# Kernel optimization log

Hardware: AMD Instinct MI355X
Metric: run time of the kernel (lower is better)

## Reference

```python
import jax, jax.numpy as jnp
import numpy as np

N = 100000   # nodes
E = 1200000  # edges
IN = 128     # in_channels
H = 64       # hidden_channels


def setup_inputs() -> dict:
    key = jax.random.key(0)
    ks = jax.random.split(key, 8)
    x = jax.random.normal(ks[0], (N, IN), jnp.float32)
    edge_index = jax.random.randint(ks[1], (2, E), 0, N, dtype=jnp.int32)
    W_pre = jax.random.normal(ks[2], (IN, H), jnp.float32) * (1.0 / np.sqrt(IN))
    b_pre = jnp.zeros((H,), jnp.float32)
    W1 = jax.random.normal(ks[3], (H, H), jnp.float32) * (1.0 / np.sqrt(H))
    b1 = jnp.zeros((H,), jnp.float32)
    W2 = jax.random.normal(ks[4], (H, H), jnp.float32) * (1.0 / np.sqrt(H))
    b2 = jnp.zeros((H,), jnp.float32)
    return {"x": x, "edge_index": edge_index, "W_pre": W_pre, "b_pre": b_pre,
            "W1": W1, "b1": b1, "W2": W2, "b2": b2}


def _gcn_conv(x, src, dst, W, b, n):
    # PyG GCNConv: x' = D^{-1/2} (A + I) D^{-1/2} (x @ W) + b
    x = x @ W                                   # [N, H]
    deg = jax.ops.segment_sum(jnp.ones_like(dst, jnp.float32), dst, num_segments=n)
    dinv = jnp.where(deg > 0, jax.lax.rsqrt(jnp.maximum(deg, 1e-12)), 0.0)
    norm = dinv[src] * dinv[dst]                # [E+N]
    msg = x[src] * norm[:, None]                # gather + scale, [E+N, H]
    out = jax.ops.segment_sum(msg, dst, num_segments=n)  # scatter-add, [N, H]
    return out + b


def reference(x, edge_index, W_pre, b_pre, W1, b1, W2, b2):
    n = x.shape[0]
    loop = jnp.arange(n, dtype=edge_index.dtype)
    # add self-loops once (same structure both layers)
    src = jnp.concatenate([edge_index[0], loop])
    dst = jnp.concatenate([edge_index[1], loop])
    x = x @ W_pre + b_pre
    ori_x = x
    x = jax.nn.relu(_gcn_conv(x, src, dst, W1, b1, n))
    x = jax.nn.relu(_gcn_conv(x, src, dst, W2, b2, n))
    return (x, ori_x)
```

## Files before the change

kernel.cpp:

```cpp
#include <hip/hip_runtime.h>

#define H 64
#define SLOTS 64
#define NPB 128
#define BSHIFT 7
#define CAP 2048
#define CHUNK 4096
#define CPAD 16

typedef __attribute__((ext_vector_type(8))) short short8;
typedef __attribute__((ext_vector_type(4))) float floatx4;
typedef __attribute__((ext_vector_type(8))) unsigned short ushort8v;

static __device__ __forceinline__ unsigned short f2bf(float f) {
  union { float f; unsigned u; } x{f};
  unsigned r = x.u + 0x7fffu + ((x.u >> 16) & 1u);
  return (unsigned short)(r >> 16);
}
static __device__ __forceinline__ float bf2f(unsigned short u) {
  union { unsigned u; float f; } x{(unsigned)u << 16};
  return x.f;
}


__global__ __launch_bounds__(512) void bucket_scatter_kernel(const int* __restrict__ src,
                                                             const int* __restrict__ dst,
                                                             int* __restrict__ gcursor,
                                                             unsigned int* __restrict__ bpk,
                                                             int E, int NB) {
  __shared__ int cnt[1024];
  __shared__ int base[1024];
  int t = threadIdx.x;
  for (int i = t; i < NB; i += 512) cnt[i] = 0;
  __syncthreads();
  int cbase = blockIdx.x * CHUNK;
  int s[CHUNK / 512], d[CHUNK / 512];
#pragma unroll
  for (int j = 0; j < CHUNK / 512; ++j) {
    int e = cbase + j * 512 + t;
    s[j] = (e < E) ? src[e] : -1;
    d[j] = (e < E) ? dst[e] : -1;
    if (d[j] >= 0) atomicAdd(&cnt[d[j] >> BSHIFT], 1);
  }
  __syncthreads();
  for (int i = t; i < NB; i += 512)
    base[i] = cnt[i] ? (i * CAP + atomicAdd(&gcursor[i * CPAD], cnt[i])) : 0;
  __syncthreads();
  for (int i = t; i < NB; i += 512) cnt[i] = 0;
  __syncthreads();
#pragma unroll
  for (int j = 0; j < CHUNK / 512; ++j) {
    if (d[j] >= 0) {
      int b = d[j] >> BSHIFT;
      int r = atomicAdd(&cnt[b], 1);
      int slot = base[b] + r;
      if (slot < (b + 1) * CAP)
        bpk[slot] = ((unsigned)s[j] << BSHIFT) | (unsigned)(d[j] & (NPB - 1));
    }
  }
}


__global__ __launch_bounds__(256) void slab_build_kernel(const unsigned int* __restrict__ bpk,
                                                         const int* __restrict__ gcursor,
                                                         int* __restrict__ csr64,
                                                         float* __restrict__ dinv, int N) {
  __shared__ int cnt[NPB];
  __shared__ int woff[NPB];
  const int b = blockIdx.x;
  const int t = threadIdx.x;
  if (t < NPB) cnt[t] = 0;
  __syncthreads();
  const int beg = b * CAP;
  const int end = beg + min(gcursor[b * CPAD], CAP);
  for (int e = beg + t; e < end; e += 256)
    atomicAdd(&cnt[bpk[e] & (NPB - 1)], 1);
  __syncthreads();

  if (t < NPB) {
    int node = b * NPB + t;
    if (node < N) {
      csr64[(size_t)node * SLOTS] = cnt[t];
      dinv[node] = rsqrtf((float)cnt[t] + 1.0f);
    }
    woff[t] = 0;
  }
  __syncthreads();

  for (int e = beg + t; e < end; e += 256) {
    unsigned pk = bpk[e];
    int nl = (int)(pk & (NPB - 1));
    int r = atomicAdd(&woff[nl], 1);
    if (r < SLOTS - 1)
      csr64[((size_t)(b * NPB + nl)) * SLOTS + 1 + r] = (int)(pk >> BSHIFT);
  }
}


__global__ __launch_bounds__(256) void wprep_kernel(const float* __restrict__ Wpre,
                                                    const float* __restrict__ W1,
                                                    const float* __restrict__ W2,
                                                    unsigned short* __restrict__ frag) {
  int i = blockIdx.x * 256 + threadIdx.x;
  const float* W;
  int K, base;
  if (i < 8192) {
    W = Wpre; K = 128; base = 0;
  } else if (i < 12288) {
    W = W1; K = 64; base = 8192;
  } else if (i < 16384) {
    W = W2; K = 64; base = 12288;
  } else {
    return;
  }
  int s = i - base;
  int j = s & 7;
  int t = s >> 3;
  int l = t & 63;
  int t2 = t >> 6;
  int KB = K / 32;
  int kb = t2 % KB;
  int w = t2 / KB;
  int k = kb * 32 + ((l >> 4) & 3) * 8 + j;
  int n = w * 16 + (l & 15);
  frag[i] = f2bf(W[k * H + n]);
}


__global__ __launch_bounds__(256) void fused_gemm_kernel(
    const float* __restrict__ X, const unsigned short* __restrict__ Wfrag,
    const float* __restrict__ bpre, const float* __restrict__ dinv,
    float* __restrict__ ori, unsigned short* __restrict__ g, int N) {
  __shared__ __align__(16) unsigned short As[4 * 64 * 8];
  __shared__ __align__(16) unsigned short os[16 * 72];
  __shared__ float dinv_s[16];
  const int tid = threadIdx.x;
  const int w = tid >> 6;
  const int lane = tid & 63;
  const int row0 = blockIdx.x * 16;

  {
    int kb = tid >> 6;
    int l = tid & 63;
    int m = l & 15;
    int k0 = kb * 32 + (l >> 4) * 8;
    int r = row0 + m;
    ushort8v v = {0, 0, 0, 0, 0, 0, 0, 0};
    if (r < N) {
      const float* xp = &X[(size_t)r * 128 + k0];
      float4 a = *(const float4*)xp;
      float4 b = *(const float4*)(xp + 4);
      v = ushort8v{f2bf(a.x), f2bf(a.y), f2bf(a.z), f2bf(a.w),
                   f2bf(b.x), f2bf(b.y), f2bf(b.z), f2bf(b.w)};
    }
    *(ushort8v*)&As[(kb * 64 + l) * 8] = v;
  }
  if (tid < 16) dinv_s[tid] = (row0 + tid < N) ? dinv[row0 + tid] : 1.f;

  short8 bfragP[4], bfrag1[2];
  {
    const unsigned short* wf = &Wfrag[((size_t)(w * 4) * 64 + lane) * 8];
#pragma unroll
    for (int kb = 0; kb < 4; ++kb) bfragP[kb] = *(const short8*)&wf[kb * 512];
    const unsigned short* wf1 = &Wfrag[8192 + ((size_t)(w * 2) * 64 + lane) * 8];
#pragma unroll
    for (int kb = 0; kb < 2; ++kb) bfrag1[kb] = *(const short8*)&wf1[kb * 512];
  }
  __syncthreads();

  floatx4 accP = {0.f, 0.f, 0.f, 0.f};
#pragma unroll
  for (int kb = 0; kb < 4; ++kb) {
    short8 a = *(const short8*)&As[(kb * 64 + lane) * 8];
    accP = __builtin_amdgcn_mfma_f32_16x16x32_bf16(a, bfragP[kb], accP, 0, 0, 0);
  }

  const int c = w * 16 + (lane & 15);
  const int q = lane >> 4;
  {
    float bv = bpre[c];
#pragma unroll
    for (int r = 0; r < 4; ++r) {
      int m = q * 4 + r;
      int row = row0 + m;
      float v = accP[r] + bv;
      if (row < N) ori[(size_t)row * H + c] = v;
      os[m * 72 + c] = f2bf(v);
    }
  }
  __syncthreads();

  floatx4 acc2 = {0.f, 0.f, 0.f, 0.f};
#pragma unroll
  for (int kb = 0; kb < 2; ++kb) {
    short8 a = *(const short8*)&os[(lane & 15) * 72 + kb * 32 + (lane >> 4) * 8];
    acc2 = __builtin_amdgcn_mfma_f32_16x16x32_bf16(a, bfrag1[kb], acc2, 0, 0, 0);
  }
#pragma unroll
  for (int r = 0; r < 4; ++r) {
    int row = row0 + q * 4 + r;
    if (row < N) g[(size_t)row * H + c] = f2bf(acc2[r] * dinv_s[q * 4 + r]);
  }
}


static __device__ __forceinline__ float gather_rows(const unsigned short* __restrict__ g,
                                                    int hv, int deg, int lane, int zrow) {
  float acc = 0.f;
#pragma unroll
  for (int b = 0; b < 4; ++b) {
    if (b * 16 < deg) {
      float x[16];
#pragma unroll
      for (int u = 0; u < 16; ++u) {
        int slot = b * 16 + 1 + u;
        int sidx = (slot < SLOTS) ? __builtin_amdgcn_readlane(hv, slot) : zrow;
        sidx = (slot <= deg) ? sidx : zrow;
        x[u] = bf2f(g[(size_t)sidx * H + lane]);
      }
#pragma unroll
      for (int u = 0; u < 16; ++u) acc += x[u];
    }
  }
  return acc;
}


__global__ __launch_bounds__(1024) void gather_fused_kernel(
    const unsigned short* __restrict__ g, const int* __restrict__ csr64,
    const float* __restrict__ bias, const unsigned short* __restrict__ w2frag,
    unsigned short* __restrict__ out, int N) {
  __shared__ __align__(16) unsigned short os[16 * 72];
  __shared__ float dinv_s[16];
  const int tid = threadIdx.x;
  const int w = tid >> 6;
  const int lane = tid & 63;
  const int node0 = blockIdx.x * 16;
  const int node = node0 + w;

  float x1 = 0.f;
  if (node < N) {
    int hv = csr64[(size_t)node * SLOTS + lane];
    float self = bf2f(g[(size_t)node * H + lane]);
    float bl = bias[lane];
    int degt = __builtin_amdgcn_readlane(hv, 0);
    float dn = rsqrtf((float)degt + 1.0f);
    int deg = min(degt, SLOTS - 1);
    float acc = self + gather_rows(g, hv, deg, lane, N);
    x1 = fmaxf(fmaf(dn, acc, bl), 0.f);
    if (lane == 0) dinv_s[w] = dn;
  }
  os[w * 72 + lane] = f2bf(x1);
  __syncthreads();

  if (w < 4) {
    short8 bfrag[2];
#pragma unroll
    for (int kb = 0; kb < 2; ++kb)
      bfrag[kb] = *(const short8*)&w2frag[((size_t)(w * 2 + kb) * 64 + lane) * 8];
    floatx4 acc2 = {0.f, 0.f, 0.f, 0.f};
#pragma unroll
    for (int kb = 0; kb < 2; ++kb) {
      short8 a = *(const short8*)&os[(lane & 15) * 72 + kb * 32 + (lane >> 4) * 8];
      acc2 = __builtin_amdgcn_mfma_f32_16x16x32_bf16(a, bfrag[kb], acc2, 0, 0, 0);
    }
    const int c = w * 16 + (lane & 15);
    const int q = lane >> 4;
#pragma unroll
    for (int r = 0; r < 4; ++r) {
      int row = node0 + q * 4 + r;
      if (row < N) out[(size_t)row * H + c] = f2bf(acc2[r] * dinv_s[q * 4 + r]);
    }
  }
}


__global__ __launch_bounds__(256) void gather_kernel(const unsigned short* __restrict__ g,
                                                     const int* __restrict__ csr64,
                                                     const float* __restrict__ bias,
                                                     float* __restrict__ out, int N) {
  int node = (blockIdx.x * 256 + threadIdx.x) >> 6;
  int c = threadIdx.x & 63;
  if (node >= N) return;

  int hv = csr64[(size_t)node * SLOTS + c];
  float self = bf2f(g[(size_t)node * H + c]);
  float bl = bias[c];
  int degt = __builtin_amdgcn_readlane(hv, 0);
  float dn = rsqrtf((float)degt + 1.0f);
  int deg = min(degt, SLOTS - 1);
  float acc = self + gather_rows(g, hv, deg, c, N);
  out[(size_t)node * H + c] = fmaxf(fmaf(dn, acc, bl), 0.f);
}


extern "C" void kernel_launch(void* const* d_in, const int* in_sizes, int n_in,
                              void* d_out, int out_size, void* d_ws, size_t ws_size,
                              hipStream_t stream) {
  const float* x = (const float*)d_in[0];
  const int* ei = (const int*)d_in[1];
  const float* W_pre = (const float*)d_in[2];
  const float* b_pre = (const float*)d_in[3];
  const float* W1 = (const float*)d_in[4];
  const float* b1 = (const float*)d_in[5];
  const float* W2 = (const float*)d_in[6];
  const float* b2 = (const float*)d_in[7];

  const int IN = 128;
  const int N = in_sizes[0] / IN;
  const int E = in_sizes[1] / 2;
  const int* src = ei;
  const int* dst = ei + E;
  const int NB = (N + NPB - 1) / NPB;

  float* out = (float*)d_out;
  float* ori = out + (size_t)N * H;

  char* p = (char*)d_ws;
  auto take = [&](size_t bytes) {
    char* q = p;
    p += (bytes + 255) & ~(size_t)255;
    return q;
  };
  int* gcursor = (int*)take(1024 * CPAD * 4);
  float* dinv = (float*)take((size_t)N * 4);
  unsigned int* bpk = (unsigned int*)take((size_t)NB * CAP * 4);
  int* csr64 = (int*)take((size_t)N * SLOTS * 4);
  unsigned short* g1 = (unsigned short*)take((size_t)(N + 1) * H * 2);
  unsigned short* g2 = (unsigned short*)take((size_t)(N + 1) * H * 2);
  unsigned short* wfrag = (unsigned short*)take(16384 * 2);

  hipMemsetAsync(gcursor, 0, (size_t)NB * CPAD * 4, stream);
  hipMemsetAsync(g1 + (size_t)N * H, 0, H * 2, stream);
  hipMemsetAsync(g2 + (size_t)N * H, 0, H * 2, stream);

  int eb = (E + CHUNK - 1) / CHUNK;
  bucket_scatter_kernel<<<eb, 512, 0, stream>>>(src, dst, gcursor, bpk, E, NB);
  slab_build_kernel<<<NB, 256, 0, stream>>>(bpk, gcursor, csr64, dinv, N);
  wprep_kernel<<<64, 256, 0, stream>>>(W_pre, W1, W2, wfrag);

  int gb = (N + 15) / 16;
  int nb = (N + 3) / 4;

  fused_gemm_kernel<<<gb, 256, 0, stream>>>(x, wfrag, b_pre, dinv, ori, g1, N);
  gather_fused_kernel<<<gb, 1024, 0, stream>>>(g1, csr64, b1, wfrag + 12288, g2, N);
  gather_kernel<<<nb, 256, 0, stream>>>(g2, csr64, b2, out, N);
}
```

Before: 234.9 us.

## Process two nodes per wavefront in gather kernels and fold weight prep into slab build

Each wavefront in both gather kernels now handles two destination nodes, issuing the first 16 neighbor-row loads for both nodes together to raise memory-level parallelism. The fused gather kernel processes 32 nodes per block and uses 8 MFMA waves for the W2 projection. The weight-fragment prep kernel is merged into slab_build as extra blocks, removing one launch. Launch bounds with occupancy hints are added, which risks register pressure from the doubled load arrays.

```diff
diff --git a/kernel.cpp b/kernel.cpp
--- a/kernel.cpp
+++ b/kernel.cpp
@@ -61,14 +61,41 @@
 }
 
 
-__global__ __launch_bounds__(256) void slab_build_kernel(const unsigned int* __restrict__ bpk,
-                                                         const int* __restrict__ gcursor,
-                                                         int* __restrict__ csr64,
-                                                         float* __restrict__ dinv, int N) {
+__global__ __launch_bounds__(256) void slab_build_kernel(
+    const unsigned int* __restrict__ bpk, const int* __restrict__ gcursor,
+    int* __restrict__ csr64, float* __restrict__ dinv, int N, int NB,
+    const float* __restrict__ Wpre, const float* __restrict__ W1,
+    const float* __restrict__ W2, unsigned short* __restrict__ frag) {
+  const int b = blockIdx.x;
+  const int t = threadIdx.x;
+  if (b >= NB) {
+    int i = (b - NB) * 256 + t;
+    if (i >= 16384) return;
+    const float* W;
+    int K, base;
+    if (i < 8192) {
+      W = Wpre; K = 128; base = 0;
+    } else if (i < 12288) {
+      W = W1; K = 64; base = 8192;
+    } else {
+      W = W2; K = 64; base = 12288;
+    }
+    int s = i - base;
+    int j = s & 7;
+    int tt = s >> 3;
+    int l = tt & 63;
+    int t2 = tt >> 6;
+    int KB = K / 32;
+    int kb = t2 % KB;
+    int w = t2 / KB;
+    int k = kb * 32 + ((l >> 4) & 3) * 8 + j;
+    int n = w * 16 + (l & 15);
+    frag[i] = f2bf(W[k * H + n]);
+    return;
+  }
+
   __shared__ int cnt[NPB];
   __shared__ int woff[NPB];
-  const int b = blockIdx.x;
-  const int t = threadIdx.x;
   if (t < NPB) cnt[t] = 0;
   __syncthreads();
   const int beg = b * CAP;
@@ -94,36 +121,6 @@
     if (r < SLOTS - 1)
       csr64[((size_t)(b * NPB + nl)) * SLOTS + 1 + r] = (int)(pk >> BSHIFT);
   }
-}
-
-
-__global__ __launch_bounds__(256) void wprep_kernel(const float* __restrict__ Wpre,
-                                                    const float* __restrict__ W1,
-                                                    const float* __restrict__ W2,
-                                                    unsigned short* __restrict__ frag) {
-  int i = blockIdx.x * 256 + threadIdx.x;
-  const float* W;
-  int K, base;
-  if (i < 8192) {
-    W = Wpre; K = 128; base = 0;
-  } else if (i < 12288) {
-    W = W1; K = 64; base = 8192;
-  } else if (i < 16384) {
-    W = W2; K = 64; base = 12288;
-  } else {
-    return;
-  }
-  int s = i - base;
-  int j = s & 7;
-  int t = s >> 3;
-  int l = t & 63;
-  int t2 = t >> 6;
-  int KB = K / 32;
-  int kb = t2 % KB;
-  int w = t2 / KB;
-  int k = kb * 32 + ((l >> 4) & 3) * 8 + j;
-  int n = w * 16 + (l & 15);
-  frag[i] = f2bf(W[k * H + n]);
 }
 
 
@@ -204,93 +201,140 @@
 }
 
 
-static __device__ __forceinline__ float gather_rows(const unsigned short* __restrict__ g,
-                                                    int hv, int deg, int lane, int zrow) {
-  float acc = 0.f;
-#pragma unroll
-  for (int b = 0; b < 4; ++b) {
-    if (b * 16 < deg) {
+static __device__ __forceinline__ void gather_rows2(
+    const unsigned short* __restrict__ g, int hvA, int hvB, int degA, int degB,
+    int lane, int zrow, float& accA, float& accB) {
+  float xa[16], xb[16];
+#pragma unroll
+  for (int u = 0; u < 16; ++u) {
+    int slot = 1 + u;
+    int s = __builtin_amdgcn_readlane(hvA, slot);
+    s = (slot <= degA) ? s : zrow;
+    xa[u] = bf2f(g[(size_t)s * H + lane]);
+  }
+#pragma unroll
+  for (int u = 0; u < 16; ++u) {
+    int slot = 1 + u;
+    int s = __builtin_amdgcn_readlane(hvB, slot);
+    s = (slot <= degB) ? s : zrow;
+    xb[u] = bf2f(g[(size_t)s * H + lane]);
+  }
+#pragma unroll
+  for (int u = 0; u < 16; ++u) accA += xa[u];
+#pragma unroll
+  for (int u = 0; u < 16; ++u) accB += xb[u];
+#pragma unroll
+  for (int b = 1; b < 4; ++b) {
+    if (b * 16 < degA) {
       float x[16];
 #pragma unroll
       for (int u = 0; u < 16; ++u) {
         int slot = b * 16 + 1 + u;
-        int sidx = (slot < SLOTS) ? __builtin_amdgcn_readlane(hv, slot) : zrow;
-        sidx = (slot <= deg) ? sidx : zrow;
-        x[u] = bf2f(g[(size_t)sidx * H + lane]);
+        int s = (slot < SLOTS) ? __builtin_amdgcn_readlane(hvA, slot) : zrow;
+        s = (slot <= degA) ? s : zrow;
+        x[u] = bf2f(g[(size_t)s * H + lane]);
       }
 #pragma unroll
-      for (int u = 0; u < 16; ++u) acc += x[u];
-    }
-  }
-  return acc;
-}
-
-
-__global__ __launch_bounds__(1024) void gather_fused_kernel(
+      for (int u = 0; u < 16; ++u) accA += x[u];
+    }
+    if (b * 16 < degB) {
+      float x[16];
+#pragma unroll
+      for (int u = 0; u < 16; ++u) {
+        int slot = b * 16 + 1 + u;
+        int s = (slot < SLOTS) ? __builtin_amdgcn_readlane(hvB, slot) : zrow;
+        s = (slot <= degB) ? s : zrow;
+        x[u] = bf2f(g[(size_t)s * H + lane]);
+      }
+#pragma unroll
+      for (int u = 0; u < 16; ++u) accB += x[u];
+    }
+  }
+}
+
+
+__global__ __launch_bounds__(1024, 8) void gather_fused_kernel(
     const unsigned short* __restrict__ g, const int* __restrict__ csr64,
     const float* __restrict__ bias, const unsigned short* __restrict__ w2frag,
     unsigned short* __restrict__ out, int N) {
-  __shared__ __align__(16) unsigned short os[16 * 72];
-  __shared__ float dinv_s[16];
+  __shared__ __align__(16) unsigned short os[32 * 72];
+  __shared__ float dinv_s[32];
   const int tid = threadIdx.x;
   const int w = tid >> 6;
   const int lane = tid & 63;
-  const int node0 = blockIdx.x * 16;
-  const int node = node0 + w;
-
-  float x1 = 0.f;
-  if (node < N) {
-    int hv = csr64[(size_t)node * SLOTS + lane];
-    float self = bf2f(g[(size_t)node * H + lane]);
-    float bl = bias[lane];
-    int degt = __builtin_amdgcn_readlane(hv, 0);
-    float dn = rsqrtf((float)degt + 1.0f);
-    int deg = min(degt, SLOTS - 1);
-    float acc = self + gather_rows(g, hv, deg, lane, N);
-    x1 = fmaxf(fmaf(dn, acc, bl), 0.f);
-    if (lane == 0) dinv_s[w] = dn;
-  }
-  os[w * 72 + lane] = f2bf(x1);
-  __syncthreads();
-
-  if (w < 4) {
+  const int node0 = blockIdx.x * 32;
+  const int nodeA = node0 + w * 2;
+  const int nodeB = nodeA + 1;
+  const bool vA = nodeA < N, vB = nodeB < N;
+
+  int hvA = vA ? csr64[(size_t)nodeA * SLOTS + lane] : 0;
+  int hvB = vB ? csr64[(size_t)nodeB * SLOTS + lane] : 0;
+  float accA = vA ? bf2f(g[(size_t)nodeA * H + lane]) : 0.f;
+  float accB = vB ? bf2f(g[(size_t)nodeB * H + lane]) : 0.f;
+  float bl = bias[lane];
+  int degtA = __builtin_amdgcn_readlane(hvA, 0);
+  int degtB = __builtin_amdgcn_readlane(hvB, 0);
+  gather_rows2(g, hvA, hvB, min(degtA, SLOTS - 1), min(degtB, SLOTS - 1),
+               lane, N, accA, accB);
+  float dnA = rsqrtf((float)degtA + 1.0f);
+  float dnB = rsqrtf((float)degtB + 1.0f);
+  os[(w * 2) * 72 + lane] = f2bf(fmaxf(fmaf(dnA, accA, bl), 0.f));
+  os[(w * 2 + 1) * 72 + lane] = f2bf(fmaxf(fmaf(dnB, accB, bl), 0.f));
+  if (lane == 0) {
+    dinv_s[w * 2] = dnA;
+    dinv_s[w * 2 + 1] = dnB;
+  }
+  __syncthreads();
+
+  if (w < 8) {
+    const int rt = w >> 2;
+    const int ct = w & 3;
     short8 bfrag[2];
 #pragma unroll
     for (int kb = 0; kb < 2; ++kb)
-      bfrag[kb] = *(const short8*)&w2frag[((size_t)(w * 2 + kb) * 64 + lane) * 8];
+      bfrag[kb] = *(const short8*)&w2frag[((size_t)(ct * 2 + kb) * 64 + lane) * 8];
     floatx4 acc2 = {0.f, 0.f, 0.f, 0.f};
 #pragma unroll
     for (int kb = 0; kb < 2; ++kb) {
-      short8 a = *(const short8*)&os[(lane & 15) * 72 + kb * 32 + (lane >> 4) * 8];
+      short8 a = *(const short8*)&os[(rt * 16 + (lane & 15)) * 72 + kb * 32 +
+                                     (lane >> 4) * 8];
       acc2 = __builtin_amdgcn_mfma_f32_16x16x32_bf16(a, bfrag[kb], acc2, 0, 0, 0);
     }
-    const int c = w * 16 + (lane & 15);
+    const int c = ct * 16 + (lane & 15);
     const int q = lane >> 4;
 #pragma unroll
     for (int r = 0; r < 4; ++r) {
-      int row = node0 + q * 4 + r;
-      if (row < N) out[(size_t)row * H + c] = f2bf(acc2[r] * dinv_s[q * 4 + r]);
-    }
-  }
-}
-
-
-__global__ __launch_bounds__(256) void gather_kernel(const unsigned short* __restrict__ g,
-                                                     const int* __restrict__ csr64,
-                                                     const float* __restrict__ bias,
-                                                     float* __restrict__ out, int N) {
-  int node = (blockIdx.x * 256 + threadIdx.x) >> 6;
+      int row = rt * 16 + q * 4 + r;
+      int node = node0 + row;
+      if (node < N) out[(size_t)node * H + c] = f2bf(acc2[r] * dinv_s[row]);
+    }
+  }
+}
+
+
+__global__ __launch_bounds__(256, 8) void gather_kernel(
+    const unsigned short* __restrict__ g, const int* __restrict__ csr64,
+    const float* __restrict__ bias, float* __restrict__ out, int N) {
+  int gw = (blockIdx.x * 256 + threadIdx.x) >> 6;
   int c = threadIdx.x & 63;
-  if (node >= N) return;
-
-  int hv = csr64[(size_t)node * SLOTS + c];
-  float self = bf2f(g[(size_t)node * H + c]);
+  int nodeA = gw * 2;
+  int nodeB = nodeA + 1;
+  if (nodeA >= N) return;
+  const bool vB = nodeB < N;
+
+  int hvA = csr64[(size_t)nodeA * SLOTS + c];
+  int hvB = vB ? csr64[(size_t)nodeB * SLOTS + c] : 0;
+  float accA = bf2f(g[(size_t)nodeA * H + c]);
+  float accB = vB ? bf2f(g[(size_t)nodeB * H + c]) : 0.f;
   float bl = bias[c];
-  int degt = __builtin_amdgcn_readlane(hv, 0);
-  float dn = rsqrtf((float)degt + 1.0f);
-  int deg = min(degt, SLOTS - 1);
-  float acc = self + gather_rows(g, hv, deg, c, N);
-  out[(size_t)node * H + c] = fmaxf(fmaf(dn, acc, bl), 0.f);
+  int degtA = __builtin_amdgcn_readlane(hvA, 0);
+  int degtB = __builtin_amdgcn_readlane(hvB, 0);
+  gather_rows2(g, hvA, hvB, min(degtA, SLOTS - 1), min(degtB, SLOTS - 1),
+               c, N, accA, accB);
+  float dnA = rsqrtf((float)degtA + 1.0f);
+  float dnB = rsqrtf((float)degtB + 1.0f);
+  out[(size_t)nodeA * H + c] = fmaxf(fmaf(dnA, accA, bl), 0.f);
+  if (vB) out[(size_t)nodeB * H + c] = fmaxf(fmaf(dnB, accB, bl), 0.f);
 }
 
 
@@ -336,13 +380,14 @@
 
   int eb = (E + CHUNK - 1) / CHUNK;
   bucket_scatter_kernel<<<eb, 512, 0, stream>>>(src, dst, gcursor, bpk, E, NB);
-  slab_build_kernel<<<NB, 256, 0, stream>>>(bpk, gcursor, csr64, dinv, N);
-  wprep_kernel<<<64, 256, 0, stream>>>(W_pre, W1, W2, wfrag);
+  slab_build_kernel<<<NB + 64, 256, 0, stream>>>(bpk, gcursor, csr64, dinv, N, NB,
+                                                 W_pre, W1, W2, wfrag);
 
   int gb = (N + 15) / 16;
-  int nb = (N + 3) / 4;
+  int gb2 = (N + 31) / 32;
+  int nb = (N + 7) / 8;
 
   fused_gemm_kernel<<<gb, 256, 0, stream>>>(x, wfrag, b_pre, dinv, ori, g1, N);
-  gather_fused_kernel<<<gb, 1024, 0, stream>>>(g1, csr64, b1, wfrag + 12288, g2, N);
+  gather_fused_kernel<<<gb2, 1024, 0, stream>>>(g1, csr64, b1, wfrag + 12288, g2, N);
   gather_kernel<<<nb, 256, 0, stream>>>(g2, csr64, b2, out, N);
 }
```

New measurement: 223.5 us. -4.9%, faster.
